# Kernel optimization log

Hardware: AMD Instinct MI355X
Metric: run time of the kernel (lower is better)

## Reference

```python
import jax, jax.numpy as jnp
import numpy as np

NH = 16      # query heads
NKV = 8      # kv heads
D = 128      # head_dim
HID = 2048   # hidden_size
EPS = 1e-6
THETA = 1e6


def _rmsnorm(x, w, eps=EPS):
    # x: [..., D]; per-head RMSNorm as in Qwen3 q_norm/k_norm
    var = jnp.mean(x * x, axis=-1, keepdims=True)
    return x * jax.lax.rsqrt(var + eps) * w


def _rope(positions, x, theta=THETA):
    # neox-style rotary (sglang get_rope default), rotary_dim == head_dim
    # x: [T, H, D]
    half = D // 2
    inv_freq = 1.0 / (theta ** (jnp.arange(half, dtype=jnp.float32) / half))
    ang = positions.astype(jnp.float32)[:, None] * inv_freq[None, :]   # [T, half]
    cos = jnp.cos(ang)[:, None, :]
    sin = jnp.sin(ang)[:, None, :]
    x1, x2 = x[..., :half], x[..., half:]
    return jnp.concatenate([x1 * cos - x2 * sin, x2 * cos + x1 * sin], axis=-1)


def setup_inputs() -> dict:
    key = jax.random.key(0)
    k1, k2, k3 = jax.random.split(key, 3)
    T = 2048
    return {
        "positions": jnp.arange(T, dtype=jnp.int32),
        "hidden_states": jax.random.normal(k1, (T, HID), dtype=jnp.float32),
        "w_qkv": jax.random.normal(k2, (HID, (NH + 2 * NKV) * D), dtype=jnp.float32) * 0.02,
        "q_norm_w": jnp.ones((D,), dtype=jnp.float32),
        "k_norm_w": jnp.ones((D,), dtype=jnp.float32),
        "w_o": jax.random.normal(k3, (NH * D, HID), dtype=jnp.float32) * 0.02,
    }


def reference(positions, hidden_states, w_qkv, q_norm_w, k_norm_w, w_o):
    T = hidden_states.shape[0]
    q_size, kv_size = NH * D, NKV * D
    qkv = hidden_states @ w_qkv                              # [T, q+2kv]
    q = qkv[:, :q_size].reshape(T, NH, D)
    k = qkv[:, q_size:q_size + kv_size].reshape(T, NKV, D)
    v = qkv[:, q_size + kv_size:].reshape(T, NKV, D)
    q = _rmsnorm(q, q_norm_w)
    k = _rmsnorm(k, k_norm_w)
    q = _rope(positions, q)
    k = _rope(positions, k)
    group = NH // NKV
    k_rep = jnp.repeat(k, group, axis=1)                     # [T, NH, D]
    v_rep = jnp.repeat(v, group, axis=1)
    scale = D ** -0.5
    scores = jnp.einsum('qhd,khd->hqk', q, k_rep) * scale    # [NH, T, T]
    causal = jnp.arange(T)[None, :] <= jnp.arange(T)[:, None]  # [q, k]
    scores = jnp.where(causal[None, :, :], scores, jnp.finfo(scores.dtype).min)
    probs = jax.nn.softmax(scores, axis=-1)
    attn = jnp.einsum('hqk,khd->qhd', probs, v_rep).reshape(T, NH * D)
    return attn @ w_o
```

## Files before the change

kernel.cpp:

```cpp
#include <hip/hip_runtime.h>
#include <cstdint>
#include <cstddef>


#define C_NH 16
#define C_NKV 8
#define C_DH 128
#define C_HID 2048
#define C_NQKV 4096
#define KVB 32

typedef unsigned short u16;
typedef __attribute__((ext_vector_type(8))) short short8;
typedef __attribute__((ext_vector_type(4))) float f32x4;

__device__ __forceinline__ u16 f2bf(float x) {
  uint32_t u = __float_as_uint(x);
  u += 0x7FFFu + ((u >> 16) & 1u);
  return (u16)(u >> 16);
}
__device__ __forceinline__ float bf2f(u16 h) {
  return __uint_as_float(((uint32_t)h) << 16);
}
__device__ __forceinline__ void bsplit(float x, u16& hi, u16& lo) {
  u16 h = f2bf(x);
  hi = h;
  lo = f2bf(x - bf2f(h));
}

__device__ __forceinline__ void gload16(const void* g, void* l) {
  __builtin_amdgcn_global_load_lds(
      (const __attribute__((address_space(1))) void*)g,
      (__attribute__((address_space(3))) void*)l, 16, 0, 0);
}

__global__ void k_trig(const int* __restrict__ pos, float2* __restrict__ tab) {
  int t = blockIdx.x;
  int j = threadIdx.x;
  float inv = 1.0f / powf(1.0e6f, (float)j * (1.0f / 64.0f));
  float ang = (float)pos[t] * inv;
  tab[t * 64 + j] = make_float2(cosf(ang), sinf(ang));
}

struct __align__(8) U4 { u16 a, b, c, d; };

__global__ void k_split(const float* __restrict__ in, u16* __restrict__ hi,
                        u16* __restrict__ lo, int n) {
  int i = (blockIdx.x * 256 + threadIdx.x) * 4;
  if (i >= n) return;
  float4 x = *(const float4*)(in + i);
  U4 hv, lv;
  bsplit(x.x, hv.a, lv.a);
  bsplit(x.y, hv.b, lv.b);
  bsplit(x.z, hv.c, lv.c);
  bsplit(x.w, hv.d, lv.d);
  *(U4*)(hi + i) = hv;
  *(U4*)(lo + i) = lv;
}

__global__ void k_split_tr(const float* __restrict__ in, u16* __restrict__ hi,
                           u16* __restrict__ lo, int K, int N) {
  __shared__ float t[64][65];
  const int kb = blockIdx.y * 64, nb = blockIdx.x * 64;
  const int tid = threadIdx.x;
  for (int i = tid; i < 4096; i += 256) {
    int r = i >> 6, c = i & 63;
    t[r][c] = in[(size_t)(kb + r) * N + nb + c];
  }
  __syncthreads();
  for (int i = tid; i < 4096; i += 256) {
    int r = i >> 6, c = i & 63;
    u16 h, l;
    bsplit(t[c][r], h, l);
    size_t o = (size_t)(nb + r) * K + kb + c;
    hi[o] = h;
    lo[o] = l;
  }
}

__global__ __launch_bounds__(256, 2)
void k_gemm_x3(const u16* __restrict__ Ah, const u16* __restrict__ Al,
               const u16* __restrict__ Bh, const u16* __restrict__ Bl,
               float* __restrict__ C, int M, int N, int K) {
  __shared__ u16 lds[4][4096];
  const int tid = threadIdx.x;
  const int lane = tid & 63;
  const int wv = tid >> 6;
  const int wr = wv >> 1, wc = wv & 1;
  const int mb = blockIdx.y * 128, nb = blockIdx.x * 128;
  const int ra = lane & 15, ko = (lane >> 4) * 8;

  f32x4 acc[4][4] = {};
  const int nk = K >> 5;
  const int rS = lane >> 2, cS = (lane & 3) * 8;

  for (int kt = 0; kt < nk; ++kt) {
    const int kb = kt * 32;
    __syncthreads();
#pragma unroll
    for (int ci = 0; ci < 2; ++ci) {
      int c = wv * 2 + ci;
      int row = c * 16 + rS;
      gload16(Ah + (size_t)(mb + row) * K + kb + cS, &lds[0][c * 512]);
      gload16(Al + (size_t)(mb + row) * K + kb + cS, &lds[1][c * 512]);
      gload16(Bh + (size_t)(nb + row) * K + kb + cS, &lds[2][c * 512]);
      gload16(Bl + (size_t)(nb + row) * K + kb + cS, &lds[3][c * 512]);
    }
    __syncthreads();

    short8 a_h[4], a_l[4], b_h[4], b_l[4];
#pragma unroll
    for (int m = 0; m < 4; ++m) {
      int r = (wr * 64 + m * 16 + ra) * 32 + ko;
      a_h[m] = *(const short8*)&lds[0][r];
      a_l[m] = *(const short8*)&lds[1][r];
    }
#pragma unroll
    for (int n = 0; n < 4; ++n) {
      int r = (wc * 64 + n * 16 + ra) * 32 + ko;
      b_h[n] = *(const short8*)&lds[2][r];
      b_l[n] = *(const short8*)&lds[3][r];
    }
#pragma unroll
    for (int m = 0; m < 4; ++m)
#pragma unroll
      for (int n = 0; n < 4; ++n) {
        acc[m][n] = __builtin_amdgcn_mfma_f32_16x16x32_bf16(a_h[m], b_h[n], acc[m][n], 0, 0, 0);
        acc[m][n] = __builtin_amdgcn_mfma_f32_16x16x32_bf16(a_h[m], b_l[n], acc[m][n], 0, 0, 0);
        acc[m][n] = __builtin_amdgcn_mfma_f32_16x16x32_bf16(a_l[m], b_h[n], acc[m][n], 0, 0, 0);
      }
  }
  const int cr = mb + wr * 64 + (lane >> 4) * 4;
  const int cc = nb + wc * 64 + ra;
#pragma unroll
  for (int m = 0; m < 4; ++m)
#pragma unroll
    for (int n = 0; n < 4; ++n)
#pragma unroll
      for (int r = 0; r < 4; ++r)
        C[(size_t)(cr + m * 16 + r) * N + cc + n * 16] = acc[m][n][r];
}

__global__ void k_normrope(const float* __restrict__ qkv, const float2* __restrict__ tab,
                           const float* __restrict__ qw, const float* __restrict__ kw,
                           u16* __restrict__ Qh, u16* __restrict__ Ql,
                           u16* __restrict__ Kh, u16* __restrict__ Kl,
                           u16* __restrict__ Vh, u16* __restrict__ Vl, int T) {
  int gw = blockIdx.x * 4 + (threadIdx.x >> 6);
  if (gw >= T * 32) return;
  int lane = threadIdx.x & 63;
  int t = gw >> 5, hd = gw & 31;
  const float* src;
  if (hd < C_NH)              src = qkv + (size_t)t * C_NQKV + hd * C_DH;
  else if (hd < C_NH + C_NKV) src = qkv + (size_t)t * C_NQKV + C_NH * C_DH + (hd - C_NH) * C_DH;
  else                        src = qkv + (size_t)t * C_NQKV + (C_NH + C_NKV) * C_DH + (hd - C_NH - C_NKV) * C_DH;
  float x1 = src[lane], x2 = src[lane + 64];

  if (hd >= C_NH + C_NKV) {
    int vh = hd - C_NH - C_NKV;
    u16 h, l;
    bsplit(x1, h, l);
    size_t o1 = ((size_t)vh * C_DH + lane) * T + t;
    Vh[o1] = h; Vl[o1] = l;
    bsplit(x2, h, l);
    size_t o2 = ((size_t)vh * C_DH + lane + 64) * T + t;
    Vh[o2] = h; Vl[o2] = l;
    return;
  }
  float ss = x1 * x1 + x2 * x2;
  ss += __shfl_xor(ss, 1, 64);
  ss += __shfl_xor(ss, 2, 64);
  ss += __shfl_xor(ss, 4, 64);
  ss += __shfl_xor(ss, 8, 64);
  ss += __shfl_xor(ss, 16, 64);
  ss += __shfl_xor(ss, 32, 64);
  float rms = rsqrtf(ss * (1.0f / 128.0f) + 1e-6f);
  const float* w = (hd < C_NH) ? qw : kw;
  float y1 = x1 * rms * w[lane];
  float y2 = x2 * rms * w[lane + 64];
  float2 cs = tab[t * 64 + lane];
  float o1 = y1 * cs.x - y2 * cs.y;
  float o2 = y2 * cs.x + y1 * cs.y;
  u16 h, l;
  if (hd < C_NH) {
    size_t o = ((size_t)t * C_NH + hd) * C_DH + lane;
    bsplit(o1, h, l); Qh[o] = h; Ql[o] = l;
    bsplit(o2, h, l); Qh[o + 64] = h; Ql[o + 64] = l;
  } else {
    int kh = hd - C_NH;
    size_t o = ((size_t)t * C_NKV + kh) * C_DH + lane;
    bsplit(o1, h, l); Kh[o] = h; Kl[o] = l;
    bsplit(o2, h, l); Kh[o + 64] = h; Kl[o + 64] = l;
  }
}

__global__ __launch_bounds__(512, 4)
void k_flash(const u16* __restrict__ Qh, const u16* __restrict__ Ql,
             const u16* __restrict__ Kg_h, const u16* __restrict__ Kg_l,
             const u16* __restrict__ Vg_h, const u16* __restrict__ Vg_l,
             u16* __restrict__ Oph, u16* __restrict__ Opl,
             float* __restrict__ Mp, float* __restrict__ Lp, int T) {
  __shared__ u16 KV[4][KVB * C_DH];
  __shared__ u16 Pex[8][2][16 * 36];
  const int tid = threadIdx.x, lane = tid & 63, wv = tid >> 6;
  const int lm = lane & 15, lq = lane >> 4;
  const int f = blockIdx.x;
  const int hk = f & 7, qt = (f >> 3) & 31, ks = f >> 8;
  const int wq = wv & 3, wh = wv >> 2;
  const int h = hk * 2 + wh;
  const int row16 = qt * 64 + wq * 16;

  short8 qfh[4], qfl[4];
#pragma unroll
  for (int kc = 0; kc < 4; ++kc) {
    size_t o = ((size_t)(row16 + lm) * C_NH + h) * C_DH + kc * 32 + lq * 8;
    qfh[kc] = *(const short8*)(Qh + o);
    qfl[kc] = *(const short8*)(Ql + o);
  }
  f32x4 o_acc[8] = {};
  float m_r[4], l_r[4];
#pragma unroll
  for (int r = 0; r < 4; ++r) { m_r[r] = -1e30f; l_r[r] = 0.f; }

  const int s_arr = wv >> 1, s_hf = wv & 1;
  const int s_rr = lane >> 4, s_ph = lane & 15;
  auto stage = [&](int kt) {
    const int kvb = kt * KVB;
#pragma unroll
    for (int j = 0; j < 4; ++j) {
      const int r0 = s_hf * 16 + j * 4;
      const int r = r0 + s_rr;
      const int c = s_ph ^ (r & 15);
      const u16* g;
      if (s_arr < 2) {
        const u16* base = (s_arr == 0) ? Kg_h : Kg_l;
        g = base + ((size_t)(kvb + r) * C_NKV + hk) * C_DH + c * 8;
      } else {
        const int d = r + ((c >> 2) << 5);
        const u16* base = (s_arr == 2) ? Vg_h : Vg_l;
        g = base + ((size_t)hk * C_DH + d) * T + kvb + (c & 3) * 8;
      }
      gload16(g, &KV[s_arr][r0 * C_DH]);
    }
  };

  const float scale = 0.08838834764831845f;
  const int nt32 = 2 * qt + 2;
  const int t0 = (ks * nt32) / 3, t1 = ((ks + 1) * nt32) / 3;

  for (int kt = t0; kt < t1; ++kt) {
    const int kvb = kt * KVB;
    stage(kt);
    __syncthreads();

    f32x4 s[2] = {};
#pragma unroll
    for (int nt = 0; nt < 2; ++nt) {
      const int krow = nt * 16 + lm;
#pragma unroll
      for (int kc = 0; kc < 4; ++kc) {
        const int phys = (kc * 4 + lq) ^ lm;
        short8 bh = *(const short8*)&KV[0][krow * C_DH + phys * 8];
        short8 bl = *(const short8*)&KV[1][krow * C_DH + phys * 8];
        s[nt] = __builtin_amdgcn_mfma_f32_16x16x32_bf16(qfh[kc], bh, s[nt], 0, 0, 0);
        s[nt] = __builtin_amdgcn_mfma_f32_16x16x32_bf16(qfh[kc], bl, s[nt], 0, 0, 0);
        s[nt] = __builtin_amdgcn_mfma_f32_16x16x32_bf16(qfl[kc], bh, s[nt], 0, 0, 0);
      }
    }

    float p[2][4];
#pragma unroll
    for (int r = 0; r < 4; ++r) {
      const int qrow = row16 + lq * 4 + r;
      float sv[2];
#pragma unroll
      for (int nt = 0; nt < 2; ++nt)
        sv[nt] = (kvb + nt * 16 + lm <= qrow) ? s[nt][r] * scale : -1e30f;
      float pm = fmaxf(sv[0], sv[1]);
      pm = fmaxf(pm, __shfl_xor(pm, 1, 16));
      pm = fmaxf(pm, __shfl_xor(pm, 2, 16));
      pm = fmaxf(pm, __shfl_xor(pm, 4, 16));
      pm = fmaxf(pm, __shfl_xor(pm, 8, 16));
      float mn = fmaxf(m_r[r], pm);
      const float safe = (mn <= -1e29f) ? 0.f : 1.f;
      float alpha = __expf(m_r[r] - mn);
      float ps = 0.f;
#pragma unroll
      for (int nt = 0; nt < 2; ++nt) {
        p[nt][r] = safe * __expf(sv[nt] - mn);
        ps += p[nt][r];
      }
      ps += __shfl_xor(ps, 1, 16);
      ps += __shfl_xor(ps, 2, 16);
      ps += __shfl_xor(ps, 4, 16);
      ps += __shfl_xor(ps, 8, 16);
      l_r[r] = l_r[r] * alpha + ps;
      m_r[r] = mn;
#pragma unroll
      for (int jb = 0; jb < 8; ++jb) o_acc[jb][r] *= alpha;
    }

#pragma unroll
    for (int r = 0; r < 4; ++r)
#pragma unroll
      for (int t2 = 0; t2 < 2; ++t2) {
        u16 ph, pl;
        bsplit(p[t2][r], ph, pl);
        Pex[wv][0][(lq * 4 + r) * 36 + t2 * 16 + lm] = ph;
        Pex[wv][1][(lq * 4 + r) * 36 + t2 * 16 + lm] = pl;
      }
    short8 pah = *(const short8*)&Pex[wv][0][lm * 36 + lq * 8];
    short8 pal = *(const short8*)&Pex[wv][1][lm * 36 + lq * 8];
#pragma unroll
    for (int jb = 0; jb < 8; ++jb) {
      const int vrow = (jb & 1) * 16 + lm;
      const int phys = ((jb >> 1) * 4 + lq) ^ lm;
      const int roff = vrow * C_DH + phys * 8;
      short8 vh = *(const short8*)&KV[2][roff];
      short8 vl = *(const short8*)&KV[3][roff];
      o_acc[jb] = __builtin_amdgcn_mfma_f32_16x16x32_bf16(pah, vh, o_acc[jb], 0, 0, 0);
      o_acc[jb] = __builtin_amdgcn_mfma_f32_16x16x32_bf16(pah, vl, o_acc[jb], 0, 0, 0);
      o_acc[jb] = __builtin_amdgcn_mfma_f32_16x16x32_bf16(pal, vh, o_acc[jb], 0, 0, 0);
    }
    __syncthreads();
  }

  const int S = T * C_NH;
#pragma unroll
  for (int r = 0; r < 4; ++r) {
    const int qrow = row16 + lq * 4 + r;
    const int rh = qrow * C_NH + h;
    if (lm == 0) { Mp[ks * S + rh] = m_r[r]; Lp[ks * S + rh] = l_r[r]; }
#pragma unroll
    for (int jb = 0; jb < 8; ++jb) {
      u16 hh, ll;
      bsplit(o_acc[jb][r], hh, ll);
      size_t oo = ((size_t)ks * S + rh) * C_DH + jb * 16 + lm;
      Oph[oo] = hh;
      Opl[oo] = ll;
    }
  }
}

__global__ void k_merge(const u16* __restrict__ Oph, const u16* __restrict__ Opl,
                        const float* __restrict__ Mp, const float* __restrict__ Lp,
                        u16* __restrict__ Oh, u16* __restrict__ Ol, int T) {
  const int idx = blockIdx.x * 256 + threadIdx.x;
  const int rh = idx >> 4, dg = idx & 15;
  const int S = T * C_NH;
  float m0 = Mp[rh], m1 = Mp[S + rh], m2 = Mp[2 * S + rh];
  float M = fmaxf(fmaxf(m0, m1), m2);
  float w0 = __expf(m0 - M), w1 = __expf(m1 - M), w2 = __expf(m2 - M);
  float L = w0 * Lp[rh] + w1 * Lp[S + rh] + w2 * Lp[2 * S + rh];
  float inv = 1.0f / L;
  const size_t b = (size_t)rh * C_DH + dg * 8;
  const size_t SO = (size_t)S * C_DH;
  short8 h0 = *(const short8*)(Oph + b),      l0 = *(const short8*)(Opl + b);
  short8 h1 = *(const short8*)(Oph + SO + b), l1 = *(const short8*)(Opl + SO + b);
  short8 h2 = *(const short8*)(Oph + 2 * SO + b), l2 = *(const short8*)(Opl + 2 * SO + b);
  short8 oh, ol;
#pragma unroll
  for (int j = 0; j < 8; ++j) {
    float o = w0 * (bf2f((u16)h0[j]) + bf2f((u16)l0[j]))
            + w1 * (bf2f((u16)h1[j]) + bf2f((u16)l1[j]))
            + w2 * (bf2f((u16)h2[j]) + bf2f((u16)l2[j]));
    u16 hh, ll;
    bsplit(o * inv, hh, ll);
    oh[j] = (short)hh;
    ol[j] = (short)ll;
  }
  *(short8*)(Oh + b) = oh;
  *(short8*)(Ol + b) = ol;
}

extern "C" void kernel_launch(void* const* d_in, const int* in_sizes, int n_in,
                              void* d_out, int out_size, void* d_ws, size_t ws_size,
                              hipStream_t stream) {
  const int*   pos  = (const int*)d_in[0];
  const float* hid  = (const float*)d_in[1];
  const float* wqkv = (const float*)d_in[2];
  const float* qnw  = (const float*)d_in[3];
  const float* knw  = (const float*)d_in[4];
  const float* wo   = (const float*)d_in[5];
  float* out = (float*)d_out;
  const int T = in_sizes[0];

  char* ws = (char*)d_ws;
  const size_t MB = 1024 * 1024;
  u16*    hid_h = (u16*)(ws);
  u16*    hid_l = (u16*)(ws + 8 * MB);
  u16*    wq_h  = (u16*)(ws + 16 * MB);
  u16*    wq_l  = (u16*)(ws + 32 * MB);
  u16*    wo_h  = (u16*)(ws + 48 * MB);
  u16*    wo_l  = (u16*)(ws + 56 * MB);
  float*  qkv   = (float*)(ws + 64 * MB);
  u16*    q_h   = (u16*)(ws + 96 * MB);
  u16*    q_l   = (u16*)(ws + 104 * MB);
  u16*    k_h   = (u16*)(ws + 112 * MB);
  u16*    k_l   = (u16*)(ws + 116 * MB);
  u16*    v_h   = (u16*)(ws + 120 * MB);
  u16*    v_l   = (u16*)(ws + 124 * MB);
  u16*    at_h  = (u16*)(ws + 128 * MB);
  u16*    at_l  = (u16*)(ws + 136 * MB);
  float2* tab   = (float2*)(ws + 144 * MB);
  u16*   Oph = (u16*)(ws + 16 * MB);
  float* Mp  = (float*)(ws + 42 * MB);
  float* Lp  = (float*)(ws + 43 * MB);
  u16*   Opl = (u16*)(ws + 64 * MB);

  k_trig<<<T, 64, 0, stream>>>(pos, tab);
  k_split<<<(T * C_HID) / 1024, 256, 0, stream>>>(hid, hid_h, hid_l, T * C_HID);
  k_split_tr<<<dim3(C_NQKV / 64, C_HID / 64), 256, 0, stream>>>(wqkv, wq_h, wq_l, C_HID, C_NQKV);
  k_split_tr<<<dim3(C_HID / 64, C_HID / 64), 256, 0, stream>>>(wo, wo_h, wo_l, C_HID, C_HID);
  k_gemm_x3<<<dim3(C_NQKV / 128, T / 128), 256, 0, stream>>>(
      hid_h, hid_l, wq_h, wq_l, qkv, T, C_NQKV, C_HID);
  k_normrope<<<(T * 32) / 4, 256, 0, stream>>>(qkv, tab, qnw, knw, q_h, q_l, k_h, k_l, v_h, v_l, T);
  k_flash<<<3 * T / 64 * C_NKV, 512, 0, stream>>>(q_h, q_l, k_h, k_l, v_h, v_l,
                                                  Oph, Opl, Mp, Lp, T);
  k_merge<<<(T * C_NH * 16) / 256, 256, 0, stream>>>(Oph, Opl, Mp, Lp, at_h, at_l, T);
  k_gemm_x3<<<dim3(C_HID / 128, T / 128), 256, 0, stream>>>(
      at_h, at_l, wo_h, wo_l, out, T, C_HID, C_HID);
}
```

Baseline: 520.6 us.

## Widen GEMM K-tile to 64 with XOR-swizzled LDS, split-K output projection, vectorize splits

The split-bf16 GEMM now loads a 64-wide K slice per iteration into an XOR-swizzled LDS layout, which halves the barrier count per K and reduces LDS bank conflicts on the fragment reads. The output projection uses split-K over two z-slices so the small 16x16 grid fills more CUs, followed by a new add kernel that sums the partials. The bf16 hi/lo split kernels now write 16-byte vectors instead of scalar or 8-byte stores. The costs are doubled LDS per block (64KB), which may limit occupancy, plus an extra partial-buffer write, read and launch for the reduction.

```diff
diff --git a/kernel.cpp b/kernel.cpp
--- a/kernel.cpp
+++ b/kernel.cpp
@@ -42,20 +42,24 @@
   tab[t * 64 + j] = make_float2(cosf(ang), sinf(ang));
 }
 
-struct __align__(8) U4 { u16 a, b, c, d; };
-
 __global__ void k_split(const float* __restrict__ in, u16* __restrict__ hi,
                         u16* __restrict__ lo, int n) {
-  int i = (blockIdx.x * 256 + threadIdx.x) * 4;
+  int i = (blockIdx.x * 256 + threadIdx.x) * 8;
   if (i >= n) return;
-  float4 x = *(const float4*)(in + i);
-  U4 hv, lv;
-  bsplit(x.x, hv.a, lv.a);
-  bsplit(x.y, hv.b, lv.b);
-  bsplit(x.z, hv.c, lv.c);
-  bsplit(x.w, hv.d, lv.d);
-  *(U4*)(hi + i) = hv;
-  *(U4*)(lo + i) = lv;
+  float4 x0 = *(const float4*)(in + i);
+  float4 x1 = *(const float4*)(in + i + 4);
+  short8 hv, lv;
+  u16 h, l;
+  bsplit(x0.x, h, l); hv[0] = (short)h; lv[0] = (short)l;
+  bsplit(x0.y, h, l); hv[1] = (short)h; lv[1] = (short)l;
+  bsplit(x0.z, h, l); hv[2] = (short)h; lv[2] = (short)l;
+  bsplit(x0.w, h, l); hv[3] = (short)h; lv[3] = (short)l;
+  bsplit(x1.x, h, l); hv[4] = (short)h; lv[4] = (short)l;
+  bsplit(x1.y, h, l); hv[5] = (short)h; lv[5] = (short)l;
+  bsplit(x1.z, h, l); hv[6] = (short)h; lv[6] = (short)l;
+  bsplit(x1.w, h, l); hv[7] = (short)h; lv[7] = (short)l;
+  *(short8*)(hi + i) = hv;
+  *(short8*)(lo + i) = lv;
 }
 
 __global__ void k_split_tr(const float* __restrict__ in, u16* __restrict__ hi,
@@ -68,69 +72,83 @@
     t[r][c] = in[(size_t)(kb + r) * N + nb + c];
   }
   __syncthreads();
-  for (int i = tid; i < 4096; i += 256) {
-    int r = i >> 6, c = i & 63;
+  for (int i = tid; i < 512; i += 256) {
+    int r = i >> 3, c0 = (i & 7) * 8;
+    short8 hv, lv;
     u16 h, l;
-    bsplit(t[c][r], h, l);
-    size_t o = (size_t)(nb + r) * K + kb + c;
-    hi[o] = h;
-    lo[o] = l;
+#pragma unroll
+    for (int j = 0; j < 8; ++j) {
+      bsplit(t[c0 + j][r], h, l);
+      hv[j] = (short)h;
+      lv[j] = (short)l;
+    }
+    size_t o = (size_t)(nb + r) * K + kb + c0;
+    *(short8*)(hi + o) = hv;
+    *(short8*)(lo + o) = lv;
   }
 }
 
 __global__ __launch_bounds__(256, 2)
 void k_gemm_x3(const u16* __restrict__ Ah, const u16* __restrict__ Al,
                const u16* __restrict__ Bh, const u16* __restrict__ Bl,
-               float* __restrict__ C, int M, int N, int K) {
-  __shared__ u16 lds[4][4096];
+               float* __restrict__ C, int M, int N, int K, int klen) {
+  __shared__ u16 lds[4][128 * 64];
   const int tid = threadIdx.x;
   const int lane = tid & 63;
   const int wv = tid >> 6;
   const int wr = wv >> 1, wc = wv & 1;
   const int mb = blockIdx.y * 128, nb = blockIdx.x * 128;
-  const int ra = lane & 15, ko = (lane >> 4) * 8;
+  const int k0 = blockIdx.z * klen;
+  float* Cz = C + (size_t)blockIdx.z * M * N;
+  const int ra = lane & 15, lq = lane >> 4;
 
   f32x4 acc[4][4] = {};
-  const int nk = K >> 5;
-  const int rS = lane >> 2, cS = (lane & 3) * 8;
+  const int nk = klen >> 6;
+  const int s_row = lane >> 3, s_pc = lane & 7;
 
   for (int kt = 0; kt < nk; ++kt) {
-    const int kb = kt * 32;
+    const int kb = k0 + kt * 64;
     __syncthreads();
 #pragma unroll
-    for (int ci = 0; ci < 2; ++ci) {
-      int c = wv * 2 + ci;
-      int row = c * 16 + rS;
-      gload16(Ah + (size_t)(mb + row) * K + kb + cS, &lds[0][c * 512]);
-      gload16(Al + (size_t)(mb + row) * K + kb + cS, &lds[1][c * 512]);
-      gload16(Bh + (size_t)(nb + row) * K + kb + cS, &lds[2][c * 512]);
-      gload16(Bl + (size_t)(nb + row) * K + kb + cS, &lds[3][c * 512]);
+    for (int ci = 0; ci < 4; ++ci) {
+      const int L = wv * 4 + ci;
+      const int row = L * 8 + s_row;
+      const int cl = s_pc ^ (row & 7);
+      gload16(Ah + (size_t)(mb + row) * K + kb + cl * 8, &lds[0][L * 512]);
+      gload16(Al + (size_t)(mb + row) * K + kb + cl * 8, &lds[1][L * 512]);
+      gload16(Bh + (size_t)(nb + row) * K + kb + cl * 8, &lds[2][L * 512]);
+      gload16(Bl + (size_t)(nb + row) * K + kb + cl * 8, &lds[3][L * 512]);
     }
     __syncthreads();
 
-    short8 a_h[4], a_l[4], b_h[4], b_l[4];
-#pragma unroll
-    for (int m = 0; m < 4; ++m) {
-      int r = (wr * 64 + m * 16 + ra) * 32 + ko;
-      a_h[m] = *(const short8*)&lds[0][r];
-      a_l[m] = *(const short8*)&lds[1][r];
-    }
-#pragma unroll
-    for (int n = 0; n < 4; ++n) {
-      int r = (wc * 64 + n * 16 + ra) * 32 + ko;
-      b_h[n] = *(const short8*)&lds[2][r];
-      b_l[n] = *(const short8*)&lds[3][r];
-    }
-#pragma unroll
-    for (int m = 0; m < 4; ++m)
+#pragma unroll
+    for (int kk = 0; kk < 2; ++kk) {
+      short8 a_h[4], a_l[4], b_h[4], b_l[4];
+#pragma unroll
+      for (int m = 0; m < 4; ++m) {
+        int r = wr * 64 + m * 16 + ra;
+        int off = r * 64 + ((kk * 4 + lq) ^ (r & 7)) * 8;
+        a_h[m] = *(const short8*)&lds[0][off];
+        a_l[m] = *(const short8*)&lds[1][off];
+      }
 #pragma unroll
       for (int n = 0; n < 4; ++n) {
-        acc[m][n] = __builtin_amdgcn_mfma_f32_16x16x32_bf16(a_h[m], b_h[n], acc[m][n], 0, 0, 0);
-        acc[m][n] = __builtin_amdgcn_mfma_f32_16x16x32_bf16(a_h[m], b_l[n], acc[m][n], 0, 0, 0);
-        acc[m][n] = __builtin_amdgcn_mfma_f32_16x16x32_bf16(a_l[m], b_h[n], acc[m][n], 0, 0, 0);
-      }
-  }
-  const int cr = mb + wr * 64 + (lane >> 4) * 4;
+        int r = wc * 64 + n * 16 + ra;
+        int off = r * 64 + ((kk * 4 + lq) ^ (r & 7)) * 8;
+        b_h[n] = *(const short8*)&lds[2][off];
+        b_l[n] = *(const short8*)&lds[3][off];
+      }
+#pragma unroll
+      for (int m = 0; m < 4; ++m)
+#pragma unroll
+        for (int n = 0; n < 4; ++n) {
+          acc[m][n] = __builtin_amdgcn_mfma_f32_16x16x32_bf16(a_h[m], b_h[n], acc[m][n], 0, 0, 0);
+          acc[m][n] = __builtin_amdgcn_mfma_f32_16x16x32_bf16(a_h[m], b_l[n], acc[m][n], 0, 0, 0);
+          acc[m][n] = __builtin_amdgcn_mfma_f32_16x16x32_bf16(a_l[m], b_h[n], acc[m][n], 0, 0, 0);
+        }
+    }
+  }
+  const int cr = mb + wr * 64 + lq * 4;
   const int cc = nb + wc * 64 + ra;
 #pragma unroll
   for (int m = 0; m < 4; ++m)
@@ -138,7 +156,17 @@
     for (int n = 0; n < 4; ++n)
 #pragma unroll
       for (int r = 0; r < 4; ++r)
-        C[(size_t)(cr + m * 16 + r) * N + cc + n * 16] = acc[m][n][r];
+        Cz[(size_t)(cr + m * 16 + r) * N + cc + n * 16] = acc[m][n][r];
+}
+
+__global__ void k_add2(const float* __restrict__ C0, const float* __restrict__ C1,
+                       float* __restrict__ out, int n) {
+  int i = (blockIdx.x * 256 + threadIdx.x) * 4;
+  if (i >= n) return;
+  float4 a = *(const float4*)(C0 + i);
+  float4 b = *(const float4*)(C1 + i);
+  a.x += b.x; a.y += b.y; a.z += b.z; a.w += b.w;
+  *(float4*)(out + i) = a;
 }
 
 __global__ void k_normrope(const float* __restrict__ qkv, const float2* __restrict__ tab,
@@ -407,17 +435,19 @@
   float* Mp  = (float*)(ws + 42 * MB);
   float* Lp  = (float*)(ws + 43 * MB);
   u16*   Opl = (u16*)(ws + 64 * MB);
+  float* Csp = (float*)(ws + 16 * MB);
 
   k_trig<<<T, 64, 0, stream>>>(pos, tab);
-  k_split<<<(T * C_HID) / 1024, 256, 0, stream>>>(hid, hid_h, hid_l, T * C_HID);
+  k_split<<<(T * C_HID) / 2048, 256, 0, stream>>>(hid, hid_h, hid_l, T * C_HID);
   k_split_tr<<<dim3(C_NQKV / 64, C_HID / 64), 256, 0, stream>>>(wqkv, wq_h, wq_l, C_HID, C_NQKV);
   k_split_tr<<<dim3(C_HID / 64, C_HID / 64), 256, 0, stream>>>(wo, wo_h, wo_l, C_HID, C_HID);
-  k_gemm_x3<<<dim3(C_NQKV / 128, T / 128), 256, 0, stream>>>(
-      hid_h, hid_l, wq_h, wq_l, qkv, T, C_NQKV, C_HID);
+  k_gemm_x3<<<dim3(C_NQKV / 128, T / 128, 1), 256, 0, stream>>>(
+      hid_h, hid_l, wq_h, wq_l, qkv, T, C_NQKV, C_HID, C_HID);
   k_normrope<<<(T * 32) / 4, 256, 0, stream>>>(qkv, tab, qnw, knw, q_h, q_l, k_h, k_l, v_h, v_l, T);
   k_flash<<<3 * T / 64 * C_NKV, 512, 0, stream>>>(q_h, q_l, k_h, k_l, v_h, v_l,
                                                   Oph, Opl, Mp, Lp, T);
   k_merge<<<(T * C_NH * 16) / 256, 256, 0, stream>>>(Oph, Opl, Mp, Lp, at_h, at_l, T);
-  k_gemm_x3<<<dim3(C_HID / 128, T / 128), 256, 0, stream>>>(
-      at_h, at_l, wo_h, wo_l, out, T, C_HID, C_HID);
-}
+  k_gemm_x3<<<dim3(C_HID / 128, T / 128, 2), 256, 0, stream>>>(
+      at_h, at_l, wo_h, wo_l, Csp, T, C_HID, C_HID, C_HID / 2);
+  k_add2<<<(T * C_HID) / 1024, 256, 0, stream>>>(Csp, Csp + (size_t)T * C_HID, out, T * C_HID);
+}
```

New measurement: 495.9 us. 1.05x faster.
